# Optimization experiments

Hardware: AMD Instinct MI355X
Metric: run time of the kernel (lower is better)

Reference implementation:

```python
import jax, jax.numpy as jnp
import numpy as np

N, C, T, V = 64, 64, 256, 25
O, R = 64, 8  # out_channels, rel_channels = in_channels // 8


def _conv1x1(x, W, b):
    # x: [N,C,T,V], W: [O,C], b: [O] -> [N,O,T,V]
    return jnp.einsum('oc,nctv->notv', W, x) + b[None, :, None, None]


def setup_inputs() -> dict:
    key = jax.random.key(0)
    ks = jax.random.split(key, 16)
    s = 0.05
    return {
        'x': jax.random.normal(ks[0], (N, C, T, V), jnp.float32),
        'A': jax.random.normal(ks[1], (V, V), jnp.float32),
        'W1': jax.random.normal(ks[2], (R, C), jnp.float32) * s,
        'b1': jnp.zeros((R,), jnp.float32),
        'W2': jax.random.normal(ks[3], (R, C), jnp.float32) * s,
        'b2': jnp.zeros((R,), jnp.float32),
        'W3': jax.random.normal(ks[4], (O, C), jnp.float32) * s,
        'b3': jnp.zeros((O,), jnp.float32),
        'W4': jax.random.normal(ks[5], (O, R), jnp.float32) * s,
        'b4': jnp.zeros((O,), jnp.float32),
        'W5': jax.random.normal(ks[6], (R, C), jnp.float32) * s,
        'b5': jnp.zeros((R,), jnp.float32),
        'w6': jax.random.normal(ks[7], (), jnp.float32),
        'b6': jnp.zeros((), jnp.float32),
        'w7': jax.random.normal(ks[8], (), jnp.float32),
        'b7': jnp.zeros((), jnp.float32),
    }


def reference(x, A, W1, b1, W2, b2, W3, b3, W4, b4, W5, b5, w6, b6, w7, b7):
    alpha = 1.0
    beta = 1.0
    # branch projections
    x1m = _conv1x1(x, W1, b1).mean(axis=2)          # [N,R,V]
    x2m = _conv1x1(x, W2, b2).mean(axis=2)          # [N,R,V]
    x3 = _conv1x1(x, W3, b3)                        # [N,O,T,V]
    # topology refinement: tanh of pairwise differences -> [N,R,V,V]
    d = jnp.tanh(x1m[:, :, :, None] - x2m[:, :, None, :])
    # per-channel attention (vectorized over the rel_channels loop).
    # q@k^T = 25 * (w6*m_u+b6)*(w7*m_v+b7); /sqrt(25) -> factor 5.
    m = _conv1x1(x, W5, b5).mean(axis=2)            # [N,R,V]
    q = w6 * m + b6
    k = w7 * m + b7
    att = 5.0 * q[:, :, :, None] * k[:, :, None, :]  # [N,R,V,V]
    res = jnp.tanh(jax.nn.softmax(att, axis=-1))     # [N,R,V,V]
    # conv4 lifts rel_channels -> out_channels on the VxV maps
    proj = lambda t: jnp.einsum('or,nruv->nouv', W4, t) + b4[None, :, None, None]
    adj = proj(d) * alpha + A[None, None, :, :] + proj(res) * beta  # [N,O,V,V]
    # aggregate: einsum('ncuv,nctv->nctu')
    return jnp.einsum('nouv,notv->notu', adj, x3)    # [N,O,T,V]
```

## Files before the change

### kernel.cpp

```cpp
#include <hip/hip_runtime.h>


#define N_ 64
#define C_ 64
#define T_ 256
#define V_ 25
#define O_ 64
#define R_ 8

#define TV_ (T_*V_)
#define XM_FLOATS (N_*C_*V_)
#define ADJ_STRIDE 28

__global__ __launch_bounds__(256) void k1_mean(const float* __restrict__ x,
                                               float* __restrict__ xm) {
  __shared__ float xl[TV_];
  __shared__ float red[4][V_];
  const int tid = threadIdx.x;
  const size_t base = (size_t)blockIdx.x * TV_;
  const float4* xg = reinterpret_cast<const float4*>(x + base);
  for (int i = tid; i < TV_/4; i += 256) {
    float4 v = xg[i];
    float* dst = &xl[4*i];
    dst[0]=v.x; dst[1]=v.y; dst[2]=v.z; dst[3]=v.w;
  }
  __syncthreads();
  float s[V_];
  #pragma unroll
  for (int v = 0; v < V_; ++v) s[v] = xl[tid*V_ + v];
  #pragma unroll
  for (int v = 0; v < V_; ++v) {
    #pragma unroll
    for (int off = 32; off >= 1; off >>= 1) s[v] += __shfl_xor(s[v], off);
  }
  const int lane = tid & 63, w = tid >> 6;
  if (lane == 0) {
    #pragma unroll
    for (int v = 0; v < V_; ++v) red[w][v] = s[v];
  }
  __syncthreads();
  if (tid < V_) {
    float t = red[0][tid] + red[1][tid] + red[2][tid] + red[3][tid];
    xm[(size_t)blockIdx.x * V_ + tid] = t * (1.0f / T_);
  }
}

__global__ __launch_bounds__(256) void kA_x3(const float* __restrict__ x,
                                             const float* __restrict__ W3,
                                             const float* __restrict__ b3,
                                             float* __restrict__ x3) {
  const int n = blockIdx.y;
  const int col = blockIdx.x * 256 + threadIdx.x;
  const size_t nbase = (size_t)n * C_ * TV_;
  float xv[C_];
  #pragma unroll
  for (int c = 0; c < C_; ++c)
    xv[c] = x[nbase + (size_t)c * TV_ + col];
  for (int o = 0; o < O_; ++o) {
    const float* wr = W3 + o * C_;
    float a0 = 0.f, a1 = 0.f, a2 = 0.f, a3 = 0.f;
    #pragma unroll
    for (int c = 0; c < C_; c += 4) {
      a0 += wr[c+0] * xv[c+0];
      a1 += wr[c+1] * xv[c+1];
      a2 += wr[c+2] * xv[c+2];
      a3 += wr[c+3] * xv[c+3];
    }
    x3[nbase + (size_t)o * TV_ + col] = (a0 + a1) + (a2 + a3) + b3[o];
  }
}

__global__ __launch_bounds__(256) void k2_adj(
    const float* __restrict__ xm, const float* __restrict__ A,
    const float* __restrict__ W1, const float* __restrict__ b1,
    const float* __restrict__ W2, const float* __restrict__ b2,
    const float* __restrict__ W4, const float* __restrict__ b4,
    const float* __restrict__ W5, const float* __restrict__ b5,
    const float* __restrict__ w6p, const float* __restrict__ b6p,
    const float* __restrict__ w7p, const float* __restrict__ b7p,
    float* __restrict__ adjP) {
  __shared__ float xmL[C_ * V_];
  __shared__ float p1[R_ * V_];
  __shared__ float p2[R_ * V_];
  __shared__ float pm[R_ * V_];
  __shared__ float dres[R_][V_][V_];
  const int n = blockIdx.x, tid = threadIdx.x;

  for (int i = tid; i < C_ * V_; i += 256) xmL[i] = xm[(size_t)n * C_ * V_ + i];
  __syncthreads();

  for (int i = tid; i < 3 * R_ * V_; i += 256) {
    const int which = i / (R_ * V_), rem = i % (R_ * V_);
    const int r = rem / V_, v = rem % V_;
    const float* W = (which == 0) ? W1 : (which == 1) ? W2 : W5;
    const float* b = (which == 0) ? b1 : (which == 1) ? b2 : b5;
    float s = b[r];
    for (int c = 0; c < C_; ++c) s += W[r * C_ + c] * xmL[c * V_ + v];
    float* P = (which == 0) ? p1 : (which == 1) ? p2 : pm;
    P[rem] = s;
  }
  __syncthreads();

  if (tid < R_ * V_) {
    const int r = tid / V_, u = tid % V_;
    const float w6 = w6p[0], b6 = b6p[0], w7 = w7p[0], b7 = b7p[0];
    const float qu = w6 * pm[r * V_ + u] + b6;
    float e[V_];
    float mx = -INFINITY;
    #pragma unroll
    for (int v = 0; v < V_; ++v) {
      float a = 5.0f * qu * (w7 * pm[r * V_ + v] + b7);
      e[v] = a;
      mx = fmaxf(mx, a);
    }
    float ssum = 0.f;
    #pragma unroll
    for (int v = 0; v < V_; ++v) { float ev = expf(e[v] - mx); e[v] = ev; ssum += ev; }
    const float inv = 1.0f / ssum;
    const float p1u = p1[r * V_ + u];
    #pragma unroll
    for (int v = 0; v < V_; ++v) {
      float res = tanhf(e[v] * inv);
      float dv  = tanhf(p1u - p2[r * V_ + v]);
      dres[r][u][v] = dv + res;
    }
  }
  __syncthreads();

  for (int i = tid; i < O_ * V_; i += 256) {
    const int o = i / V_, u = i % V_;
    const float b4o2 = 2.0f * b4[o];
    float w4r[R_];
    #pragma unroll
    for (int r = 0; r < R_; ++r) w4r[r] = W4[o * R_ + r];
    float* dst = adjP + ((size_t)(n * O_ + o) * V_ + u) * ADJ_STRIDE;
    #pragma unroll
    for (int v = 0; v < V_; ++v) {
      float s = b4o2 + A[u * V_ + v];
      #pragma unroll
      for (int r = 0; r < R_; ++r) s += w4r[r] * dres[r][u][v];
      dst[v] = s;
    }
  }
}

__global__ __launch_bounds__(256) void kB_out(float* __restrict__ x3,
                                              const float* __restrict__ adjP) {
  __shared__ float tl[T_ * 26];
  __shared__ __align__(16) float adjL[V_ * ADJ_STRIDE];
  const int o = blockIdx.x, n = blockIdx.y;
  const int tid = threadIdx.x;
  float* g = x3 + (size_t)(n * O_ + o) * TV_;

  const float4* g4 = reinterpret_cast<const float4*>(g);
  for (int i = tid; i < TV_/4; i += 256) {
    float4 v = g4[i];
    const int f = 4 * i;
    #pragma unroll
    for (int e = 0; e < 4; ++e) {
      const int fe = f + e;
      tl[(fe / V_) * 26 + (fe % V_)] = (&v.x)[e];
    }
  }
  if (tid < 175) {
    float4 a = reinterpret_cast<const float4*>(adjP + (size_t)(n * O_ + o) * (V_ * ADJ_STRIDE))[tid];
    float* d = &adjL[4 * tid];
    d[0]=a.x; d[1]=a.y; d[2]=a.z; d[3]=a.w;
  }
  __syncthreads();

  float xr[V_];
  #pragma unroll
  for (int v = 0; v < V_; ++v) xr[v] = tl[tid * 26 + v];
  float orr[V_];
  #pragma unroll
  for (int u = 0; u < V_; ++u) {
    const float* ar = &adjL[u * ADJ_STRIDE];
    float s = 0.f;
    #pragma unroll
    for (int j = 0; j < 6; ++j) {
      float4 a = *reinterpret_cast<const float4*>(ar + 4 * j);
      s += a.x * xr[4*j] + a.y * xr[4*j+1] + a.z * xr[4*j+2] + a.w * xr[4*j+3];
    }
    s += ar[24] * xr[24];
    orr[u] = s;
  }
  __syncthreads();
  #pragma unroll
  for (int u = 0; u < V_; ++u) tl[tid * 26 + u] = orr[u];
  __syncthreads();
  for (int i = tid; i < TV_/4; i += 256) {
    const int f = 4 * i;
    float4 v;
    #pragma unroll
    for (int e = 0; e < 4; ++e) {
      const int fe = f + e;
      (&v.x)[e] = tl[(fe / V_) * 26 + (fe % V_)];
    }
    reinterpret_cast<float4*>(g)[i] = v;
  }
}

extern "C" void kernel_launch(void* const* d_in, const int* in_sizes, int n_in,
                              void* d_out, int out_size, void* d_ws, size_t ws_size,
                              hipStream_t stream) {
  const float* x  = (const float*)d_in[0];
  const float* A  = (const float*)d_in[1];
  const float* W1 = (const float*)d_in[2];
  const float* b1 = (const float*)d_in[3];
  const float* W2 = (const float*)d_in[4];
  const float* b2 = (const float*)d_in[5];
  const float* W3 = (const float*)d_in[6];
  const float* b3 = (const float*)d_in[7];
  const float* W4 = (const float*)d_in[8];
  const float* b4 = (const float*)d_in[9];
  const float* W5 = (const float*)d_in[10];
  const float* b5 = (const float*)d_in[11];
  const float* w6 = (const float*)d_in[12];
  const float* b6 = (const float*)d_in[13];
  const float* w7 = (const float*)d_in[14];
  const float* b7 = (const float*)d_in[15];
  float* out  = (float*)d_out;
  float* xm   = (float*)d_ws;
  float* adjP = xm + XM_FLOATS;

  k1_mean<<<dim3(N_ * C_), 256, 0, stream>>>(x, xm);
  kA_x3 <<<dim3(TV_ / 256, N_), 256, 0, stream>>>(x, W3, b3, out);
  k2_adj<<<dim3(N_), 256, 0, stream>>>(xm, A, W1, b1, W2, b2, W4, b4, W5, b5,
                                       w6, b6, w7, b7, adjP);
  kB_out<<<dim3(O_, N_), 256, 0, stream>>>(out, adjP);
}
```

Baseline: 426.0 us.

## Fuse x3 projection with adjacency aggregation to avoid x3 round trip

Replaces the separate conv3 kernel and the aggregation kernel with one fused kernel. Each block handles a tile of 8 time steps for one batch and computes x3 for 4 output channels at a time into shared memory. It then immediately applies the V x V adjacency and writes the final output. This removes writing x3 to global memory and reading it back. In exchange, 7 of every 32 lanes are idle because V=25 is padded to 32, each o-step needs extra barriers, and the adjacency is reloaded per block.

Result: slower. 445.6 us (+4.6%).

```diff
diff --git a/kernel.cpp b/kernel.cpp
--- a/kernel.cpp
+++ b/kernel.cpp
@@ -11,6 +11,7 @@
 #define TV_ (T_*V_)
 #define XM_FLOATS (N_*C_*V_)
 #define ADJ_STRIDE 28
+#define ADJ_ROW (V_*ADJ_STRIDE)
 
 __global__ __launch_bounds__(256) void k1_mean(const float* __restrict__ x,
                                                float* __restrict__ xm) {
@@ -42,31 +43,6 @@
   if (tid < V_) {
     float t = red[0][tid] + red[1][tid] + red[2][tid] + red[3][tid];
     xm[(size_t)blockIdx.x * V_ + tid] = t * (1.0f / T_);
-  }
-}
-
-__global__ __launch_bounds__(256) void kA_x3(const float* __restrict__ x,
-                                             const float* __restrict__ W3,
-                                             const float* __restrict__ b3,
-                                             float* __restrict__ x3) {
-  const int n = blockIdx.y;
-  const int col = blockIdx.x * 256 + threadIdx.x;
-  const size_t nbase = (size_t)n * C_ * TV_;
-  float xv[C_];
-  #pragma unroll
-  for (int c = 0; c < C_; ++c)
-    xv[c] = x[nbase + (size_t)c * TV_ + col];
-  for (int o = 0; o < O_; ++o) {
-    const float* wr = W3 + o * C_;
-    float a0 = 0.f, a1 = 0.f, a2 = 0.f, a3 = 0.f;
-    #pragma unroll
-    for (int c = 0; c < C_; c += 4) {
-      a0 += wr[c+0] * xv[c+0];
-      a1 += wr[c+1] * xv[c+1];
-      a2 += wr[c+2] * xv[c+2];
-      a3 += wr[c+3] * xv[c+3];
-    }
-    x3[nbase + (size_t)o * TV_ + col] = (a0 + a1) + (a2 + a3) + b3[o];
   }
 }
 
@@ -133,7 +109,7 @@
     float w4r[R_];
     #pragma unroll
     for (int r = 0; r < R_; ++r) w4r[r] = W4[o * R_ + r];
-    float* dst = adjP + ((size_t)(n * O_ + o) * V_ + u) * ADJ_STRIDE;
+    float* dst = adjP + (size_t)(n * O_ + o) * ADJ_ROW + (size_t)u * ADJ_STRIDE;
     #pragma unroll
     for (int v = 0; v < V_; ++v) {
       float s = b4o2 + A[u * V_ + v];
@@ -144,60 +120,74 @@
   }
 }
 
-__global__ __launch_bounds__(256) void kB_out(float* __restrict__ x3,
-                                              const float* __restrict__ adjP) {
-  __shared__ float tl[T_ * 26];
-  __shared__ __align__(16) float adjL[V_ * ADJ_STRIDE];
-  const int o = blockIdx.x, n = blockIdx.y;
+#define TT 8
+#define OSTEP 4
+__global__ __launch_bounds__(256, 4) void kF(const float* __restrict__ x,
+                                             const float* __restrict__ W3,
+                                             const float* __restrict__ b3,
+                                             const float* __restrict__ adjP,
+                                             float* __restrict__ out) {
+  __shared__ float x3L[OSTEP][TT][32];
+  __shared__ __align__(16) float adjL[OSTEP][ADJ_ROW];
   const int tid = threadIdx.x;
-  float* g = x3 + (size_t)(n * O_ + o) * TV_;
-
-  const float4* g4 = reinterpret_cast<const float4*>(g);
-  for (int i = tid; i < TV_/4; i += 256) {
-    float4 v = g4[i];
-    const int f = 4 * i;
-    #pragma unroll
-    for (int e = 0; e < 4; ++e) {
-      const int fe = f + e;
-      tl[(fe / V_) * 26 + (fe % V_)] = (&v.x)[e];
-    }
-  }
-  if (tid < 175) {
-    float4 a = reinterpret_cast<const float4*>(adjP + (size_t)(n * O_ + o) * (V_ * ADJ_STRIDE))[tid];
-    float* d = &adjL[4 * tid];
-    d[0]=a.x; d[1]=a.y; d[2]=a.z; d[3]=a.w;
-  }
-  __syncthreads();
-
-  float xr[V_];
+  const int t  = tid >> 5;
+  const int vp = tid & 31;
+  const int n  = blockIdx.y;
+  const int t0 = blockIdx.x * TT;
+  const size_t nbase = (size_t)n * C_ * TV_;
+  const int vclamp = (vp < V_) ? vp : (V_ - 1);
+  const int col = (t0 + t) * V_ + vclamp;
+
+  float xv[C_];
   #pragma unroll
-  for (int v = 0; v < V_; ++v) xr[v] = tl[tid * 26 + v];
-  float orr[V_];
-  #pragma unroll
-  for (int u = 0; u < V_; ++u) {
-    const float* ar = &adjL[u * ADJ_STRIDE];
-    float s = 0.f;
-    #pragma unroll
-    for (int j = 0; j < 6; ++j) {
-      float4 a = *reinterpret_cast<const float4*>(ar + 4 * j);
-      s += a.x * xr[4*j] + a.y * xr[4*j+1] + a.z * xr[4*j+2] + a.w * xr[4*j+3];
-    }
-    s += ar[24] * xr[24];
-    orr[u] = s;
-  }
-  __syncthreads();
-  #pragma unroll
-  for (int u = 0; u < V_; ++u) tl[tid * 26 + u] = orr[u];
-  __syncthreads();
-  for (int i = tid; i < TV_/4; i += 256) {
-    const int f = 4 * i;
-    float4 v;
-    #pragma unroll
-    for (int e = 0; e < 4; ++e) {
-      const int fe = f + e;
-      (&v.x)[e] = tl[(fe / V_) * 26 + (fe % V_)];
-    }
-    reinterpret_cast<float4*>(g)[i] = v;
+  for (int c = 0; c < C_; ++c) xv[c] = x[nbase + (size_t)c * TV_ + col];
+
+  const float* adjN = adjP + (size_t)n * O_ * ADJ_ROW;
+  const bool active_u = (vp < V_);
+  const int ui = active_u ? vp : 0;
+
+  for (int op = 0; op < O_; op += OSTEP) {
+    float4 a[OSTEP];
+    if (tid < ADJ_ROW / 4) {
+      #pragma unroll
+      for (int k = 0; k < OSTEP; ++k)
+        a[k] = reinterpret_cast<const float4*>(adjN + (size_t)(op + k) * ADJ_ROW)[tid];
+    }
+    #pragma unroll
+    for (int k = 0; k < OSTEP; ++k) {
+      const float* wr = W3 + (op + k) * C_;
+      float s0 = 0.f, s1 = 0.f, s2 = 0.f, s3 = 0.f;
+      #pragma unroll
+      for (int c = 0; c < C_; c += 4) {
+        s0 += wr[c+0] * xv[c+0];
+        s1 += wr[c+1] * xv[c+1];
+        s2 += wr[c+2] * xv[c+2];
+        s3 += wr[c+3] * xv[c+3];
+      }
+      x3L[k][t][vp] = (s0 + s1) + (s2 + s3) + b3[op + k];
+    }
+    if (tid < ADJ_ROW / 4) {
+      #pragma unroll
+      for (int k = 0; k < OSTEP; ++k)
+        reinterpret_cast<float4*>(&adjL[k][0])[tid] = a[k];
+    }
+    __syncthreads();
+    #pragma unroll
+    for (int k = 0; k < OSTEP; ++k) {
+      const float* ar = &adjL[k][ui * ADJ_STRIDE];
+      const float* xr = &x3L[k][t][0];
+      float acc = 0.f;
+      #pragma unroll
+      for (int j = 0; j < 6; ++j) {
+        float4 av = *reinterpret_cast<const float4*>(ar + 4 * j);
+        float4 xw = *reinterpret_cast<const float4*>(xr + 4 * j);
+        acc += av.x * xw.x + av.y * xw.y + av.z * xw.z + av.w * xw.w;
+      }
+      acc += ar[24] * xr[24];
+      if (active_u)
+        out[nbase + (size_t)(op + k) * TV_ + (size_t)(t0 + t) * V_ + vp] = acc;
+    }
+    __syncthreads();
   }
 }
 
@@ -225,8 +215,7 @@
   float* adjP = xm + XM_FLOATS;
 
   k1_mean<<<dim3(N_ * C_), 256, 0, stream>>>(x, xm);
-  kA_x3 <<<dim3(TV_ / 256, N_), 256, 0, stream>>>(x, W3, b3, out);
   k2_adj<<<dim3(N_), 256, 0, stream>>>(xm, A, W1, b1, W2, b2, W4, b4, W5, b5,
                                        w6, b6, w7, b7, adjP);
-  kB_out<<<dim3(O_, N_), 256, 0, stream>>>(out, adjP);
-}
+  kF<<<dim3(T_ / TT, N_), 256, 0, stream>>>(x, W3, b3, adjP, out);
+}
```
